# Kernel tuning notes

Hardware: AMD Instinct MI355X
Metric: run time of the kernel (lower is better)

Reference implementation:

```python
import jax, jax.numpy as jnp
import numpy as np

V = 50257  # vocab_size
H = 512    # d_model
S = 512    # source length
B = 8      # batch
T = 64     # decode steps


def setup_inputs() -> dict:
    key = jax.random.key(0)
    k1, k2, k3, k4, k5, k6 = jax.random.split(key, 6)
    src_full = jax.random.randint(k1, (S, B), 0, V, dtype=jnp.int32)
    decode_output = jax.random.normal(k2, (T, B, H), dtype=jnp.float32)
    decode_attn = jax.random.uniform(k3, (B, T, S), dtype=jnp.float32)
    memory = jax.random.normal(k4, (S, B, H), dtype=jnp.float32)
    # learned params: gen_proj (H->V) and prob_proj (H->1)
    W_gen = jax.random.normal(k5, (H, V), dtype=jnp.float32) / np.sqrt(H)
    b_gen = jnp.zeros((V,), dtype=jnp.float32)
    W_prob = jax.random.normal(k6, (H, 1), dtype=jnp.float32) / np.sqrt(H)
    b_prob = jnp.zeros((1,), dtype=jnp.float32)
    return {
        "src_full": src_full,
        "decode_output": decode_output,
        "decode_attn": decode_attn,
        "memory": memory,
        "W_gen": W_gen,
        "b_gen": b_gen,
        "W_prob": W_prob,
        "b_prob": b_prob,
    }


def reference(src_full, decode_output, decode_attn, memory, W_gen, b_gen, W_prob, b_prob):
    # context[t,b,h] = sum_s attn[b,t,s] * memory[s,b,h]
    context = jnp.einsum("bts,sbh->tbh", decode_attn, memory)  # [T,B,H]
    prob = jax.nn.sigmoid(context @ W_prob + b_prob)           # [T,B,1] copy gate p_gen
    gen_logits = prob * jax.nn.softmax(decode_output @ W_gen + b_gen, axis=-1)  # [T,B,V]

    # scatter-add attention mass onto vocab slots: copy[t,b, src_full[s,b]] += attn[b,t,s]
    attn_tbs = jnp.transpose(decode_attn, (1, 0, 2))  # [T,B,S]
    idx = src_full.T                                  # [B,S]
    ti = jnp.arange(T)[:, None, None]
    bi = jnp.arange(B)[None, :, None]
    copy_logits = jnp.zeros((T, B, V), dtype=decode_attn.dtype).at[ti, bi, idx[None, :, :]].add(attn_tbs)
    copy_logits = (1.0 - prob) * jax.nn.softmax(copy_logits, axis=-1)

    return jnp.log(gen_logits + copy_logits)
```

## Files before the change

kernel.cpp:

```cpp
#include <hip/hip_runtime.h>
#include <hip/hip_bf16.h>
#include <math.h>

#define VV 50257
#define VP 50304
#define HH 512
#define SS 512
#define BB 8
#define TT 64
#define MM (TT*BB)

typedef __bf16 bf16x2 __attribute__((ext_vector_type(2)));
typedef __bf16 bf16x4 __attribute__((ext_vector_type(4)));
typedef __bf16 bf16x8 __attribute__((ext_vector_type(8)));
typedef float  f32x4  __attribute__((ext_vector_type(4)));

__device__ __forceinline__ __bf16 f2b(float f) {
    unsigned u = __builtin_bit_cast(unsigned, f);
    unsigned r = (u + 0x7fffu + ((u >> 16) & 1u)) >> 16;
    unsigned short s = (unsigned short)r;
    return __builtin_bit_cast(__bf16, s);
}

__device__ __forceinline__ void gl2lds16(const void* g, void* l) {
    __builtin_amdgcn_global_load_lds(
        (const __attribute__((address_space(1))) unsigned*)g,
        (__attribute__((address_space(3))) unsigned*)l, 16, 0, 0);
}

#define WAITV(n) asm volatile("s_waitcnt vmcnt(" #n ")" ::: "memory")

__global__ __launch_bounds__(256) void k_pre(const float* __restrict__ A,
                                             __bf16* __restrict__ Ab,
                                             const float* __restrict__ mem,
                                             const float* __restrict__ Wp,
                                             float* __restrict__ mw) {
    int tid = threadIdx.x;
    if (blockIdx.x < 256) {
        int i = (blockIdx.x * 256 + tid) * 4;
        float4 v = *(const float4*)&A[i];
        bf16x4 o = {f2b(v.x), f2b(v.y), f2b(v.z), f2b(v.w)};
        *(bf16x4*)&Ab[i] = o;
    } else {
        int bx = blockIdx.x - 256;
        int row = bx * 4 + (tid >> 6);
        int lane = tid & 63;
        const float* mp = mem + (size_t)row * HH;
        float acc = 0.f;
#pragma unroll
        for (int i = 0; i < HH / 64; i++)
            acc += mp[lane + 64 * i] * Wp[lane + 64 * i];
#pragma unroll
        for (int off = 32; off > 0; off >>= 1) acc += __shfl_down(acc, off);
        if (lane == 0) mw[row] = acc;
    }
}

__global__ __launch_bounds__(256) void k_mid(const float* __restrict__ attn,
                                             const float* __restrict__ mw,
                                             const float* __restrict__ bp,
                                             float* __restrict__ prob,
                                             float* __restrict__ Z,
                                             const float* __restrict__ W,
                                             __bf16* __restrict__ Wt) {
    __shared__ float tile[64][65];
    int tid = threadIdx.x;
    if (blockIdx.x < 512) {
        int r = blockIdx.x;
        int t = r / BB, b = r % BB;
        const float* ap = attn + ((size_t)b * TT + t) * SS;
        float acc = ap[tid] * mw[tid * BB + b] +
                    ap[tid + 256] * mw[(tid + 256) * BB + b];
        float* red = &tile[0][0];
        red[tid] = acc; __syncthreads();
        for (int st = 128; st > 0; st >>= 1) {
            if (tid < st) red[tid] += red[tid + st];
            __syncthreads();
        }
        if (tid == 0) {
            prob[r] = 1.f / (1.f + expf(-(red[0] + bp[0])));
            Z[r] = 0.f;
        }
    } else {
        int bx = blockIdx.x - 512;
        int n0 = (bx % (VP / 64)) * 64;
        int k0 = (bx / (VP / 64)) * 64;
#pragma unroll
        for (int i = 0; i < 16; i++) {
            int idx = tid + i * 256;
            int kk = idx >> 6, nn = idx & 63;
            int n = n0 + nn;
            tile[kk][nn] = (n < VV) ? W[(size_t)(k0 + kk) * VV + n] : 0.f;
        }
        __syncthreads();
#pragma unroll
        for (int i = 0; i < 8; i++) {
            int idx = tid + i * 256;
            int nn = idx >> 5, kp = idx & 31;
            bf16x2 o = {f2b(tile[2 * kp][nn]), f2b(tile[2 * kp + 1][nn])};
            *(bf16x2*)&Wt[(size_t)(n0 + nn) * HH + k0 + 2 * kp] = o;
        }
    }
}

template<bool BF16OUT>
__global__ __launch_bounds__(512, 4) void k_gemm4(const __bf16* __restrict__ Ab,
                                                  const __bf16* __restrict__ Wt,
                                                  const float* __restrict__ bias,
                                                  float* __restrict__ Cf,
                                                  __bf16* __restrict__ Cb,
                                                  float* __restrict__ Zrow) {
    __shared__ __bf16 As[4][4096];
    __shared__ __bf16 Bs[4][4096];
    __shared__ float zred[128];

    const int tid  = threadIdx.x;
    const int lane = tid & 63;
    const int wave = tid >> 6;
    const int l15  = lane & 15;
    const int quad = lane >> 4;
    const int wr = (wave >> 2) * 64;
    const int wc = (wave & 3) * 32;

    int L = blockIdx.x + gridDim.x * blockIdx.y;
    int xcd = L & 7, i8 = L >> 3;
    int nid = (xcd < 4 ? xcd * 197 : 4 * 197 + (xcd - 4) * 196) + i8;
    const int row0 = (nid & 3) * 128;
    const int col0 = (nid >> 2) * 128;

    const size_t offA = (size_t)(row0 + wave * 16 + l15) * HH + quad * 8;
    const size_t offB = (size_t)(col0 + wave * 16 + l15) * HH + quad * 8;

#define STAGE(buf, k0)                                   \
    do {                                                 \
        gl2lds16(Ab + offA + (k0), &As[buf][wave * 512]); \
        gl2lds16(Wt + offB + (k0), &Bs[buf][wave * 512]); \
    } while (0)

    f32x4 acc[4][2] = {};

    STAGE(0, 0);
    STAGE(1, 32);
    STAGE(2, 64);
#pragma unroll
    for (int it = 0; it < 16; ++it) {
        if (it <= 13)      WAITV(4);
        else if (it == 14) WAITV(2);
        else               WAITV(0);
        __builtin_amdgcn_s_barrier();
        if (it < 13) STAGE((it + 3) & 3, (it + 3) * 32);
        const __bf16* Al = &As[it & 3][0];
        const __bf16* Bl = &Bs[it & 3][0];
        bf16x8 af[4], bfv[2];
#pragma unroll
        for (int mt = 0; mt < 4; mt++)
            af[mt] = *(const bf16x8*)&Al[((wr >> 4) + mt) * 512 + lane * 8];
#pragma unroll
        for (int nt = 0; nt < 2; nt++)
            bfv[nt] = *(const bf16x8*)&Bl[((wc >> 4) + nt) * 512 + lane * 8];
#pragma unroll
        for (int mt = 0; mt < 4; mt++)
#pragma unroll
            for (int nt = 0; nt < 2; nt++)
                acc[mt][nt] = __builtin_amdgcn_mfma_f32_16x16x32_bf16(
                    af[mt], bfv[nt], acc[mt][nt], 0, 0, 0);
    }
#undef STAGE

    __syncthreads();
    if (tid < 128) zred[tid] = 0.f;
    __syncthreads();

#pragma unroll
    for (int mt = 0; mt < 4; mt++) {
        float esum[4] = {0.f, 0.f, 0.f, 0.f};
#pragma unroll
        for (int nt = 0; nt < 2; nt++) {
            int c = col0 + wc + nt * 16 + l15;
            if (c < VV) {
                float bv = bias[c];
#pragma unroll
                for (int i = 0; i < 4; i++) {
                    int r = row0 + wr + mt * 16 + quad * 4 + i;
                    float l = acc[mt][nt][i] + bv;
                    if (BF16OUT) Cb[(size_t)r * VP + c] = f2b(l);
                    else         Cf[(size_t)r * VV + c] = l;
                    esum[i] += __expf(l);
                }
            }
        }
#pragma unroll
        for (int i = 0; i < 4; i++) {
            float e = esum[i];
            e += __shfl_xor(e, 1);
            e += __shfl_xor(e, 2);
            e += __shfl_xor(e, 4);
            e += __shfl_xor(e, 8);
            if (l15 == 0)
                atomicAdd(&zred[wr + mt * 16 + quad * 4 + i], e);
        }
    }
    __syncthreads();
    if (tid < 128) atomicAdd(&Zrow[row0 + tid], zred[tid]);
}

#define HT 1024
#define NBW 1572

__device__ __forceinline__ void build_hash(const int* __restrict__ src,
                                           const float* __restrict__ ap,
                                           int b, int tid,
                                           int* keys, float* vals, unsigned* bmap,
                                           float* red, int* s_D, float* s_Zc) {
    for (int i = tid; i < HT; i += 256) { keys[i] = -1; vals[i] = 0.f; }
    for (int i = tid; i < NBW; i += 256) bmap[i] = 0u;
    if (tid == 0) *s_D = 0;
    __syncthreads();

    for (int s = tid; s < SS; s += 256) {
        int idx = src[s * BB + b];
        float v = ap[s];
        unsigned h = ((unsigned)idx * 2654435761u) >> 22;
        while (true) {
            int old = atomicCAS(&keys[h], -1, idx);
            if (old == -1 || old == idx) { atomicAdd(&vals[h], v); break; }
            h = (h + 1) & (HT - 1);
        }
    }
    __syncthreads();

    float lsum = 0.f; int dloc = 0;
    for (int i = tid; i < HT; i += 256) {
        int k = keys[i];
        if (k != -1) {
            lsum += __expf(vals[i]); dloc++;
            atomicOr(&bmap[(unsigned)k >> 5], 1u << (k & 31));
        }
    }
    atomicAdd(s_D, dloc);
    red[tid] = lsum; __syncthreads();
    for (int st = 128; st > 0; st >>= 1) {
        if (tid < st) red[tid] += red[tid + st];
        __syncthreads();
    }
    if (tid == 0) *s_Zc = (float)(VV - *s_D) + red[0];
    __syncthreads();
}

__global__ __launch_bounds__(1024) void k_final_row(const int* __restrict__ src,
                                                    const float* __restrict__ attn,
                                                    const float* __restrict__ prob,
                                                    const float* __restrict__ Zrow,
                                                    const __bf16* __restrict__ LG,
                                                    float* __restrict__ out) {
    __shared__ int      keys[HT];
    __shared__ float    vals[HT];
    __shared__ unsigned bmap[NBW];
    __shared__ float    red[1024];
    __shared__ int      s_D;
    __shared__ float    s_Zc;

    int r = blockIdx.x;
    int t = r / BB, b = r % BB;
    int tid = threadIdx.x;
    const float* ap = attn + ((size_t)b * TT + t) * SS;

    { int i = tid; keys[i] = -1; vals[i] = 0.f; }
    for (int i = tid; i < NBW; i += 1024) bmap[i] = 0u;
    if (tid == 0) s_D = 0;
    __syncthreads();

    if (tid < SS) {
        int idx = src[tid * BB + b];
        float v = ap[tid];
        unsigned h = ((unsigned)idx * 2654435761u) >> 22;
        while (true) {
            int old = atomicCAS(&keys[h], -1, idx);
            if (old == -1 || old == idx) { atomicAdd(&vals[h], v); break; }
            h = (h + 1) & (HT - 1);
        }
    }
    __syncthreads();

    float lsum = 0.f;
    {
        int k = keys[tid];
        bool occ = (k != -1);
        if (occ) {
            lsum = __expf(vals[tid]);
            atomicOr(&bmap[(unsigned)k >> 5], 1u << (k & 31));
        }
        unsigned long long m = __ballot(occ);
        if ((tid & 63) == 0) atomicAdd(&s_D, __popcll(m));
    }
    red[tid] = lsum; __syncthreads();
    for (int st = 512; st > 0; st >>= 1) {
        if (tid < st) red[tid] += red[tid + st];
        __syncthreads();
    }
    if (tid == 0) s_Zc = (float)(VV - s_D) + red[0];
    __syncthreads();

    float p = prob[r];
    float pinvZ = p / Zrow[r];
    float qinvZc = (1.f - p) / s_Zc;

    const __bf16* lrow = LG + (size_t)r * VP;
    float* orow = out + (size_t)r * VV;

    for (int v0 = tid * 8; v0 < VP; v0 += 8192) {
        bf16x8 l8 = *(const bf16x8*)&lrow[v0];
#pragma unroll
        for (int e = 0; e < 8; e++) {
            int v = v0 + e;
            if (v < VV) {
                float l = (float)l8[e];
                float c = 1.f;
                if ((bmap[v >> 5] >> (v & 31)) & 1u) {
                    unsigned h = ((unsigned)v * 2654435761u) >> 22;
                    while (true) {
                        int k = keys[h];
                        if (k == v) { c = __expf(vals[h]); break; }
                        if (k == -1) break;
                        h = (h + 1) & (HT - 1);
                    }
                }
                orow[v] = __logf(pinvZ * __expf(l) + qinvZc * c);
            }
        }
    }
}

#define CHUNKS 6283
__global__ __launch_bounds__(256) void k_final_s(const int* __restrict__ src,
                                                 const float* __restrict__ attn,
                                                 const float* __restrict__ prob,
                                                 const float* __restrict__ Zrow,
                                                 float* __restrict__ out) {
    __shared__ int      keys[HT];
    __shared__ float    vals[HT];
    __shared__ unsigned bmap[NBW];
    __shared__ float    red[256];
    __shared__ int      s_D;
    __shared__ float    s_Zc;

    int r = blockIdx.y;
    int t = r / BB, b = r % BB;
    int tid = threadIdx.x;
    const float* ap = attn + ((size_t)b * TT + t) * SS;
    build_hash(src, ap, b, tid, keys, vals, bmap, red, &s_D, &s_Zc);

    float p = prob[r];
    float pinvZ = p / Zrow[r];
    float qinvZc = (1.f - p) / s_Zc;

    int c0 = blockIdx.x * CHUNKS;
    int c1 = c0 + CHUNKS; if (c1 > VV) c1 = VV;
    float* rowp = out + (size_t)r * VV;

    for (int v = c0 + tid; v < c1; v += 256) {
        float l = rowp[v];
        float c = 1.f;
        if ((bmap[v >> 5] >> (v & 31)) & 1u) {
            unsigned h = ((unsigned)v * 2654435761u) >> 22;
            while (true) {
                int k = keys[h];
                if (k == v) { c = __expf(vals[h]); break; }
                if (k == -1) break;
                h = (h + 1) & (HT - 1);
            }
        }
        rowp[v] = __logf(pinvZ * __expf(l) + qinvZc * c);
    }
}

extern "C" void kernel_launch(void* const* d_in, const int* in_sizes, int n_in,
                              void* d_out, int out_size, void* d_ws, size_t ws_size,
                              hipStream_t stream) {
    const int*   src_full      = (const int*)d_in[0];
    const float* decode_output = (const float*)d_in[1];
    const float* decode_attn   = (const float*)d_in[2];
    const float* memory        = (const float*)d_in[3];
    const float* W_gen         = (const float*)d_in[4];
    const float* b_gen         = (const float*)d_in[5];
    const float* W_prob        = (const float*)d_in[6];
    const float* b_prob        = (const float*)d_in[7];
    float* out = (float*)d_out;

    float* ws   = (float*)d_ws;
    float* mw   = ws;
    float* prob = ws + 4096;
    float* Z    = ws + 4608;
    __bf16* Ab  = (__bf16*)(ws + 5120);
    __bf16* Wt  = (__bf16*)(ws + 5120 + 131072);
    __bf16* LG  = Wt + (size_t)VP * HH;

    size_t base_b = (size_t)(5120 + 131072) * sizeof(float);
    size_t wt_b   = (size_t)VP * HH * 2;
    size_t lg_b   = (size_t)MM * VP * 2;
    bool full = ws_size >= base_b + wt_b + lg_b;

    k_pre<<<1280, 256, 0, stream>>>(decode_output, Ab, memory, W_prob, mw);
    k_mid<<<512 + (VP / 64) * (HH / 64), 256, 0, stream>>>(
        decode_attn, mw, b_prob, prob, Z, W_gen, Wt);

    dim3 ggrid(MM / 128, VP / 128);
    if (full) {
        k_gemm4<true><<<ggrid, 512, 0, stream>>>(Ab, Wt, b_gen, nullptr, LG, Z);
        k_final_row<<<MM, 1024, 0, stream>>>(src_full, decode_attn, prob, Z, LG, out);
    } else {
        k_gemm4<false><<<ggrid, 512, 0, stream>>>(Ab, Wt, b_gen, out, nullptr, Z);
        dim3 fgrid((VV + CHUNKS - 1) / CHUNKS, MM);
        k_final_s<<<fgrid, 256, 0, stream>>>(src_full, decode_attn, prob, Z, out);
    }
}
```

Baseline: 355.3 us.

## Restructure weight transpose, shrink GEMM pipeline to 3 stages, split final pass

Each weight-transpose block now covers 32 vocab columns across the full K range, staging them in LDS so it can write whole 1 KB bf16 rows of Wt in 16-byte stores. The GEMM moves from a 4-stage to a 3-stage LDS ring with launch bounds raised to 6 blocks per CU, and MFMA sections run at raised wave priority. The final log-mix pass is split into two blocks per row, each covering half the vocab, and takes a fast path when none of 8 consecutive slots holds a source token. In exchange, each final block rebuilds the per-row hash table, doubling that setup, and the shallower prefetch may expose more memory latency.

```diff
diff --git a/kernel.cpp b/kernel.cpp
--- a/kernel.cpp
+++ b/kernel.cpp
@@ -56,17 +56,43 @@
     }
 }
 
-__global__ __launch_bounds__(256) void k_mid(const float* __restrict__ attn,
-                                             const float* __restrict__ mw,
-                                             const float* __restrict__ bp,
-                                             float* __restrict__ prob,
-                                             float* __restrict__ Z,
-                                             const float* __restrict__ W,
-                                             __bf16* __restrict__ Wt) {
-    __shared__ float tile[64][65];
+__global__ __launch_bounds__(256) void k_wt(const float* __restrict__ W,
+                                            __bf16* __restrict__ Wt,
+                                            const float* __restrict__ attn,
+                                            const float* __restrict__ mw,
+                                            const float* __restrict__ bp,
+                                            float* __restrict__ prob,
+                                            float* __restrict__ Z) {
+    __shared__ float tile[32][33];
+    __shared__ __bf16 Wo[32][520];
     int tid = threadIdx.x;
-    if (blockIdx.x < 512) {
-        int r = blockIdx.x;
+
+    if (blockIdx.x < VP / 32) {
+        int n0 = blockIdx.x * 32;
+        int nn = tid >> 3, ks = (tid & 7) * 4;
+        for (int kc = 0; kc < 16; kc++) {
+            int k0 = kc * 32;
+#pragma unroll
+            for (int rd = 0; rd < 4; rd++) {
+                int idx = rd * 256 + tid;
+                int kk = idx >> 5, nc = idx & 31;
+                int n = n0 + nc;
+                tile[kk][nc] = (n < VV) ? W[(size_t)(k0 + kk) * VV + n] : 0.f;
+            }
+            __syncthreads();
+            bf16x4 o = {f2b(tile[ks][nn]), f2b(tile[ks + 1][nn]),
+                        f2b(tile[ks + 2][nn]), f2b(tile[ks + 3][nn])};
+            *(bf16x4*)&Wo[nn][k0 + ks] = o;
+            __syncthreads();
+        }
+#pragma unroll
+        for (int i = 0; i < 8; i++) {
+            int r = i * 4 + (tid >> 6);
+            int c = (tid & 63) * 8;
+            *(bf16x8*)&Wt[(size_t)(n0 + r) * HH + c] = *(const bf16x8*)&Wo[r][c];
+        }
+    } else {
+        int r = blockIdx.x - VP / 32;
         int t = r / BB, b = r % BB;
         const float* ap = attn + ((size_t)b * TT + t) * SS;
         float acc = ap[tid] * mw[tid * BB + b] +
@@ -81,37 +107,18 @@
             prob[r] = 1.f / (1.f + expf(-(red[0] + bp[0])));
             Z[r] = 0.f;
         }
-    } else {
-        int bx = blockIdx.x - 512;
-        int n0 = (bx % (VP / 64)) * 64;
-        int k0 = (bx / (VP / 64)) * 64;
-#pragma unroll
-        for (int i = 0; i < 16; i++) {
-            int idx = tid + i * 256;
-            int kk = idx >> 6, nn = idx & 63;
-            int n = n0 + nn;
-            tile[kk][nn] = (n < VV) ? W[(size_t)(k0 + kk) * VV + n] : 0.f;
-        }
-        __syncthreads();
-#pragma unroll
-        for (int i = 0; i < 8; i++) {
-            int idx = tid + i * 256;
-            int nn = idx >> 5, kp = idx & 31;
-            bf16x2 o = {f2b(tile[2 * kp][nn]), f2b(tile[2 * kp + 1][nn])};
-            *(bf16x2*)&Wt[(size_t)(n0 + nn) * HH + k0 + 2 * kp] = o;
-        }
     }
 }
 
 template<bool BF16OUT>
-__global__ __launch_bounds__(512, 4) void k_gemm4(const __bf16* __restrict__ Ab,
+__global__ __launch_bounds__(512, 6) void k_gemm5(const __bf16* __restrict__ Ab,
                                                   const __bf16* __restrict__ Wt,
                                                   const float* __restrict__ bias,
                                                   float* __restrict__ Cf,
                                                   __bf16* __restrict__ Cb,
                                                   float* __restrict__ Zrow) {
-    __shared__ __bf16 As[4][4096];
-    __shared__ __bf16 Bs[4][4096];
+    __shared__ __bf16 As[3][4096];
+    __shared__ __bf16 Bs[3][4096];
     __shared__ float zred[128];
 
     const int tid  = threadIdx.x;
@@ -131,8 +138,8 @@
     const size_t offA = (size_t)(row0 + wave * 16 + l15) * HH + quad * 8;
     const size_t offB = (size_t)(col0 + wave * 16 + l15) * HH + quad * 8;
 
-#define STAGE(buf, k0)                                   \
-    do {                                                 \
+#define STAGE(buf, k0)                                    \
+    do {                                                  \
         gl2lds16(Ab + offA + (k0), &As[buf][wave * 512]); \
         gl2lds16(Wt + offB + (k0), &Bs[buf][wave * 512]); \
     } while (0)
@@ -141,16 +148,14 @@
 
     STAGE(0, 0);
     STAGE(1, 32);
-    STAGE(2, 64);
 #pragma unroll
     for (int it = 0; it < 16; ++it) {
-        if (it <= 13)      WAITV(4);
-        else if (it == 14) WAITV(2);
-        else               WAITV(0);
+        if (it < 15) WAITV(2);
+        else         WAITV(0);
         __builtin_amdgcn_s_barrier();
-        if (it < 13) STAGE((it + 3) & 3, (it + 3) * 32);
-        const __bf16* Al = &As[it & 3][0];
-        const __bf16* Bl = &Bs[it & 3][0];
+        if (it < 14) STAGE((it + 2) % 3, (it + 2) * 32);
+        const __bf16* Al = &As[it % 3][0];
+        const __bf16* Bl = &Bs[it % 3][0];
         bf16x8 af[4], bfv[2];
 #pragma unroll
         for (int mt = 0; mt < 4; mt++)
@@ -158,12 +163,14 @@
 #pragma unroll
         for (int nt = 0; nt < 2; nt++)
             bfv[nt] = *(const bf16x8*)&Bl[((wc >> 4) + nt) * 512 + lane * 8];
+        __builtin_amdgcn_s_setprio(1);
 #pragma unroll
         for (int mt = 0; mt < 4; mt++)
 #pragma unroll
             for (int nt = 0; nt < 2; nt++)
                 acc[mt][nt] = __builtin_amdgcn_mfma_f32_16x16x32_bf16(
                     af[mt], bfv[nt], acc[mt][nt], 0, 0, 0);
+        __builtin_amdgcn_s_setprio(0);
     }
 #undef STAGE
 
@@ -247,12 +254,13 @@
     __syncthreads();
 }
 
-__global__ __launch_bounds__(1024) void k_final_row(const int* __restrict__ src,
-                                                    const float* __restrict__ attn,
-                                                    const float* __restrict__ prob,
-                                                    const float* __restrict__ Zrow,
-                                                    const __bf16* __restrict__ LG,
-                                                    float* __restrict__ out) {
+#define HV (VP / 2)
+__global__ __launch_bounds__(1024) void k_final2(const int* __restrict__ src,
+                                                 const float* __restrict__ attn,
+                                                 const float* __restrict__ prob,
+                                                 const float* __restrict__ Zrow,
+                                                 const __bf16* __restrict__ LG,
+                                                 float* __restrict__ out) {
     __shared__ int      keys[HT];
     __shared__ float    vals[HT];
     __shared__ unsigned bmap[NBW];
@@ -260,12 +268,13 @@
     __shared__ int      s_D;
     __shared__ float    s_Zc;
 
-    int r = blockIdx.x;
+    int r = blockIdx.y;
+    int half = blockIdx.x;
     int t = r / BB, b = r % BB;
     int tid = threadIdx.x;
     const float* ap = attn + ((size_t)b * TT + t) * SS;
 
-    { int i = tid; keys[i] = -1; vals[i] = 0.f; }
+    { keys[tid] = -1; vals[tid] = 0.f; }
     for (int i = tid; i < NBW; i += 1024) bmap[i] = 0u;
     if (tid == 0) s_D = 0;
     __syncthreads();
@@ -308,24 +317,32 @@
     const __bf16* lrow = LG + (size_t)r * VP;
     float* orow = out + (size_t)r * VV;
 
-    for (int v0 = tid * 8; v0 < VP; v0 += 8192) {
+    int base = half * HV;
+    for (int v0 = base + tid * 8; v0 < base + HV; v0 += 8192) {
         bf16x8 l8 = *(const bf16x8*)&lrow[v0];
-#pragma unroll
-        for (int e = 0; e < 8; e++) {
-            int v = v0 + e;
-            if (v < VV) {
-                float l = (float)l8[e];
-                float c = 1.f;
-                if ((bmap[v >> 5] >> (v & 31)) & 1u) {
-                    unsigned h = ((unsigned)v * 2654435761u) >> 22;
-                    while (true) {
-                        int k = keys[h];
-                        if (k == v) { c = __expf(vals[h]); break; }
-                        if (k == -1) break;
-                        h = (h + 1) & (HT - 1);
+        unsigned bits = (bmap[v0 >> 5] >> (v0 & 31)) & 0xFFu;
+        if (bits == 0u && v0 + 8 <= VV) {
+#pragma unroll
+            for (int e = 0; e < 8; e++)
+                orow[v0 + e] = __logf(pinvZ * __expf((float)l8[e]) + qinvZc);
+        } else {
+#pragma unroll
+            for (int e = 0; e < 8; e++) {
+                int v = v0 + e;
+                if (v < VV) {
+                    float l = (float)l8[e];
+                    float c = 1.f;
+                    if ((bits >> e) & 1u) {
+                        unsigned h = ((unsigned)v * 2654435761u) >> 22;
+                        while (true) {
+                            int k = keys[h];
+                            if (k == v) { c = __expf(vals[h]); break; }
+                            if (k == -1) break;
+                            h = (h + 1) & (HT - 1);
+                        }
                     }
+                    orow[v] = __logf(pinvZ * __expf(l) + qinvZc * c);
                 }
-                orow[v] = __logf(pinvZ * __expf(l) + qinvZc * c);
             }
         }
     }
@@ -401,15 +418,16 @@
     bool full = ws_size >= base_b + wt_b + lg_b;
 
     k_pre<<<1280, 256, 0, stream>>>(decode_output, Ab, memory, W_prob, mw);
-    k_mid<<<512 + (VP / 64) * (HH / 64), 256, 0, stream>>>(
-        decode_attn, mw, b_prob, prob, Z, W_gen, Wt);
+    k_wt<<<VP / 32 + 512, 256, 0, stream>>>(W_gen, Wt, decode_attn, mw, b_prob,
+                                            prob, Z);
 
     dim3 ggrid(MM / 128, VP / 128);
     if (full) {
-        k_gemm4<true><<<ggrid, 512, 0, stream>>>(Ab, Wt, b_gen, nullptr, LG, Z);
-        k_final_row<<<MM, 1024, 0, stream>>>(src_full, decode_attn, prob, Z, LG, out);
+        k_gemm5<true><<<ggrid, 512, 0, stream>>>(Ab, Wt, b_gen, nullptr, LG, Z);
+        dim3 fgrid(2, MM);
+        k_final2<<<fgrid, 1024, 0, stream>>>(src_full, decode_attn, prob, Z, LG, out);
     } else {
-        k_gemm4<false><<<ggrid, 512, 0, stream>>>(Ab, Wt, b_gen, out, nullptr, Z);
+        k_gemm5<false><<<ggrid, 512, 0, stream>>>(Ab, Wt, b_gen, out, nullptr, Z);
         dim3 fgrid((VV + CHUNKS - 1) / CHUNKS, MM);
         k_final_s<<<fgrid, 256, 0, stream>>>(src_full, decode_attn, prob, Z, out);
     }
```

After: 328.9 us. 1.08x faster.
